# Kernel optimization log

Hardware: AMD Instinct MI355X
Metric: run time of the kernel (lower is better)

## Reference

```python
import jax, jax.numpy as jnp
import numpy as np

NUM_EXPERTS = 8
TOP_K = 2


def setup_inputs() -> dict:
    key = jax.random.key(0)
    ks = jax.random.split(key, 6)
    D, H, E = 1024, 4096, NUM_EXPERTS
    B, S = 4, 2048
    s = 0.02
    return {
        "x": jax.random.normal(ks[0], (B, S, D), jnp.float32),
        "scale_embeddings": jax.random.normal(ks[1], (10, D), jnp.float32) * s,
        "router_w": jax.random.normal(ks[2], (E, D), jnp.float32) * s,
        "router_b": jnp.zeros((E,), jnp.float32),
        "fc1_w": jax.random.normal(ks[3], (E, H, D), jnp.float32) * s,
        "fc1_b": jnp.zeros((E, H), jnp.float32),
        "fc2_w": jax.random.normal(ks[4], (E, D, H), jnp.float32) * s,
        "fc2_b": jnp.zeros((E, D), jnp.float32),
        "scale_idx": 3,
    }


def reference(x, scale_embeddings, router_w, router_b, fc1_w, fc1_b, fc2_w, fc2_b, scale_idx):
    B, S, D = x.shape
    T = B * S
    # Scale-aware router (eval mode: no jitter, temperature=1.0).
    xs = x + scale_embeddings[scale_idx][None, None, :]
    logits = jnp.einsum('bsd,ed->bse', xs, router_w) + router_b  # [B,S,E]
    top_w, top_idx = jax.lax.top_k(logits, TOP_K)                 # [B,S,K]
    top_w = jax.nn.softmax(top_w, axis=-1)

    # Dense per-expert FFN (tanh-approx GELU), then gather top-k expert outputs.
    xf = x.reshape(T, D)
    outs = []
    for e in range(NUM_EXPERTS):
        h = jax.nn.gelu(xf @ fc1_w[e].T + fc1_b[e], approximate=True)  # [T,H]
        outs.append(h @ fc2_w[e].T + fc2_b[e])                          # [T,D]
    all_out = jnp.stack(outs)                                           # [E,T,D]

    idx_f = top_idx.reshape(T, TOP_K)
    w_f = top_w.reshape(T, TOP_K)
    gathered = all_out[idx_f, jnp.arange(T)[:, None]]  # [T,K,D]
    out = (gathered * w_f[..., None]).sum(axis=1)      # [T,D]
    return out.reshape(B, S, D)
```

## Files before the change

### kernel.cpp

```cpp
#include <hip/hip_runtime.h>
#include <math.h>

#define TTOK 8192
#define DDIM 1024
#define HDIM 4096
#define NEXP 8
#define NASSIGN (TTOK * 2)

typedef float f32x4 __attribute__((ext_vector_type(4)));
typedef short s16x8 __attribute__((ext_vector_type(8)));

__device__ __forceinline__ unsigned short f2bf(float f) {
  union { float f; unsigned int u; } v; v.f = f;
  unsigned int u = v.u;
  u += 0x7FFFu + ((u >> 16) & 1u);
  return (unsigned short)(u >> 16);
}

__device__ __forceinline__ float gelu_fast(float x) {
  float u = 0.7978845608028654f * x * (1.0f + 0.044715f * x * x);
  return x / (1.0f + __expf(-2.0f * u));
}

__global__ void cvt_bf16_k(const float* __restrict__ w1, unsigned short* __restrict__ w1b,
                           const float* __restrict__ w2, unsigned short* __restrict__ w2b,
                           int n8) {
  int i = blockIdx.x * blockDim.x + threadIdx.x;
  const float* src; unsigned short* dst;
  if (i < n8) { src = w1; dst = w1b; } else { src = w2; dst = w2b; i -= n8; }
#pragma unroll
  for (int c = 0; c < 2; ++c) {
    float4 v = ((const float4*)src)[i * 2 + c];
    ushort4 o;
    o.x = f2bf(v.x); o.y = f2bf(v.y); o.z = f2bf(v.z); o.w = f2bf(v.w);
    ((ushort4*)dst)[i * 2 + c] = o;
  }
}

__global__ void router_k(const float* __restrict__ x, const float* __restrict__ se,
                         const int* __restrict__ sidx, const float* __restrict__ rw,
                         const float* __restrict__ rb,
                         int* __restrict__ e0, int* __restrict__ e1,
                         float* __restrict__ w0, float* __restrict__ w1,
                         int* __restrict__ counts) {
  int t = blockIdx.x * 4 + (threadIdx.x >> 6);
  int lane = threadIdx.x & 63;
  const float4* xp = (const float4*)(x + (size_t)t * DDIM) + lane * 4;
  const float4* sp = (const float4*)(se + (size_t)sidx[0] * DDIM) + lane * 4;
  float xs[16];
#pragma unroll
  for (int c = 0; c < 4; ++c) {
    float4 a = xp[c], b = sp[c];
    xs[c * 4 + 0] = a.x + b.x; xs[c * 4 + 1] = a.y + b.y;
    xs[c * 4 + 2] = a.z + b.z; xs[c * 4 + 3] = a.w + b.w;
  }
  double acc[NEXP];
#pragma unroll
  for (int e = 0; e < NEXP; ++e) acc[e] = 0.0;
#pragma unroll
  for (int e = 0; e < NEXP; ++e) {
    const float4* wp = (const float4*)(rw + (size_t)e * DDIM) + lane * 4;
#pragma unroll
    for (int c = 0; c < 4; ++c) {
      float4 wv = wp[c];
      acc[e] += (double)xs[c * 4 + 0] * wv.x + (double)xs[c * 4 + 1] * wv.y +
                (double)xs[c * 4 + 2] * wv.z + (double)xs[c * 4 + 3] * wv.w;
    }
  }
#pragma unroll
  for (int e = 0; e < NEXP; ++e) {
#pragma unroll
    for (int m = 32; m >= 1; m >>= 1) acc[e] += __shfl_xor(acc[e], m, 64);
  }
  if (lane == 0) {
    float lg[NEXP];
    for (int e = 0; e < NEXP; ++e) lg[e] = (float)acc[e] + rb[e];
    int i0 = 0; float l0 = lg[0];
    for (int e = 1; e < NEXP; ++e) if (lg[e] > l0) { l0 = lg[e]; i0 = e; }
    int i1 = -1; float l1 = -1e30f;
    for (int e = 0; e < NEXP; ++e) if (e != i0 && lg[e] > l1) { l1 = lg[e]; i1 = e; }
    float z = expf(l1 - l0);
    float p0 = 1.0f / (1.0f + z);
    e0[t] = i0; e1[t] = i1; w0[t] = p0; w1[t] = 1.0f - p0;
    atomicAdd(&counts[i0], 1);
    atomicAdd(&counts[i1], 1);
  }
}

__global__ void scan_k(const int* __restrict__ counts, int* __restrict__ offsets,
                       int* __restrict__ cursors, int4* __restrict__ tileT,
                       int* __restrict__ ntiles) {
  if (threadIdx.x == 0 && blockIdx.x == 0) {
    int s = 0;
    for (int e = 0; e < NEXP; ++e) { offsets[e] = s; cursors[e] = s; s += counts[e]; }
    offsets[NEXP] = s;
    int nt = 0;
    for (int e = 0; e < NEXP; ++e)
      for (int m0 = offsets[e]; m0 < offsets[e + 1]; m0 += 256)
        tileT[nt++] = make_int4(m0, offsets[e + 1], e, 0);
    ntiles[0] = nt;
  }
}

__global__ void scatter_k(const int* __restrict__ e0, const int* __restrict__ e1,
                          const float* __restrict__ w0, const float* __restrict__ w1,
                          int* __restrict__ cursors, int* __restrict__ buckets,
                          float* __restrict__ wts, int* __restrict__ s0,
                          int* __restrict__ s1) {
  int t = blockIdx.x * blockDim.x + threadIdx.x;
  if (t >= TTOK) return;
  int a = e0[t];
  int p = atomicAdd(&cursors[a], 1);
  buckets[p] = t; wts[p] = w0[t]; s0[t] = p;
  a = e1[t];
  p = atomicAdd(&cursors[a], 1);
  buckets[p] = t; wts[p] = w1[t]; s1[t] = p;
}

__global__ void gather_k(const float* __restrict__ x, const int* __restrict__ buckets,
                         unsigned short* __restrict__ Xg) {
  int r = blockIdx.x;
  int t = buckets[r];
  int i = threadIdx.x;
  float4 v = ((const float4*)(x + (size_t)t * DDIM))[i];
  ushort4 o;
  o.x = f2bf(v.x); o.y = f2bf(v.y); o.z = f2bf(v.z); o.w = f2bf(v.w);
  ((ushort4*)(Xg + (size_t)r * DDIM))[i] = o;
}


#define ASP1(p) (const __attribute__((address_space(1))) void*)(p)
#define ASP3(p) (__attribute__((address_space(3))) void*)(p)

#define STAGE_A(KT, H) do {                                                   \
    int kk_ = (KT); if (kk_ >= NKT) kk_ = NKT - 1;                            \
    const int k0_ = kk_ * 64;                                                 \
    unsigned short* d_ = (((KT) & 1) ? LA1 : LA0) + ((H) * 128 + w * 8) * 64; \
    __builtin_amdgcn_global_load_lds(ASP1(aptr[(H) * 2 + 0] + k0_), ASP3(d_), 16, 0, 0);        \
    __builtin_amdgcn_global_load_lds(ASP1(aptr[(H) * 2 + 1] + k0_), ASP3(d_ + 4096), 16, 0, 0); \
  } while (0)

#define STAGE_B(KT, H) do {                                                   \
    int kk_ = (KT); if (kk_ >= NKT) kk_ = NKT - 1;                            \
    const int k0_ = kk_ * 64;                                                 \
    unsigned short* d_ = (((KT) & 1) ? LB1 : LB0) + ((H) * 128 + w * 8) * 64; \
    __builtin_amdgcn_global_load_lds(ASP1(bptr[(H) * 2 + 0] + k0_), ASP3(d_), 16, 0, 0);        \
    __builtin_amdgcn_global_load_lds(ASP1(bptr[(H) * 2 + 1] + k0_), ASP3(d_ + 4096), 16, 0, 0); \
  } while (0)

#define PH(SL, QD, RB, STG) do {                                              \
    if (RB) {                                                                 \
      _Pragma("unroll") for (int nj_ = 0; nj_ < 4; ++nj_)                     \
      _Pragma("unroll") for (int ks_ = 0; ks_ < 2; ++ks_)                     \
        bfrag[nj_][ks_] = *(const s16x8*)(((SL) ? LB1 : LB0) +                \
            (wn * 64 + nj_ * 16 + c16) * 64 + (((ks_ * 4 + q) ^ cx) * 8));    \
    }                                                                         \
    s16x8 afr_[2][2];                                                         \
    _Pragma("unroll") for (int m2_ = 0; m2_ < 2; ++m2_)                       \
    _Pragma("unroll") for (int ks_ = 0; ks_ < 2; ++ks_)                       \
      afr_[m2_][ks_] = *(const s16x8*)(((SL) ? LA1 : LA0) +                   \
          (wm * 128 + ((QD) * 2 + m2_) * 16 + c16) * 64 +                     \
          (((ks_ * 4 + q) ^ cx) * 8));                                        \
    STG;                                                                      \
    asm volatile("s_barrier" ::: "memory");                                   \
    asm volatile("s_waitcnt lgkmcnt(0)" ::: "memory");                        \
    __builtin_amdgcn_sched_barrier(0);                                        \
    __builtin_amdgcn_s_setprio(1);                                            \
    _Pragma("unroll") for (int m2_ = 0; m2_ < 2; ++m2_)                       \
    _Pragma("unroll") for (int nj_ = 0; nj_ < 4; ++nj_)                       \
    _Pragma("unroll") for (int ks_ = 0; ks_ < 2; ++ks_)                       \
      acc[(QD) * 2 + m2_][nj_] = __builtin_amdgcn_mfma_f32_16x16x32_bf16(     \
          afr_[m2_][ks_], bfrag[nj_][ks_], acc[(QD) * 2 + m2_][nj_], 0, 0, 0);\
    __builtin_amdgcn_s_setprio(0);                                            \
  } while (0)

#define BARS asm volatile("s_barrier" ::: "memory")
#define VM4  asm volatile("s_waitcnt vmcnt(4)" ::: "memory")

template <int KD, int ND, int EPI>
__global__ __launch_bounds__(512, 2) void moe_gemm8_k(
    const unsigned short* __restrict__ A,
    const unsigned short* __restrict__ W,
    const float* __restrict__ bias,
    const int4* __restrict__ tileT, const int* __restrict__ ntiles,
    unsigned short* __restrict__ Hout, float* __restrict__ Yout) {
  constexpr int NTN = ND / 256;
  constexpr int NKT = KD / 64;
  extern __shared__ unsigned short lds[];
  unsigned short* const LA0 = lds;
  unsigned short* const LA1 = lds + 16384;
  unsigned short* const LB0 = lds + 32768;
  unsigned short* const LB1 = lds + 49152;

  const int tid = threadIdx.x;
  const int lane = tid & 63;
  const int w = tid >> 6;
  const int wm = w >> 2;
  const int wn = w & 3;
  const int q = lane >> 4;
  const int c16 = lane & 15;
  const int cx = lane & 7;
  const int l8 = lane >> 3;
  const int swz = cx ^ l8;

  const int ntm = ntiles[0];
  const int total = ntm * NTN;
  const int xcd = blockIdx.x & 7;
  const int lid = blockIdx.x >> 3;
  const int bstride = gridDim.x >> 3;
  const int per = (total + 7) >> 3;
  int begin = xcd * per;
  int end = begin + per; if (end > total) end = total;

  for (int idx = begin + lid; idx < end; idx += bstride) {
    const int nb = idx / ntm;
    const int mt = idx - nb * ntm;
    const int4 tl = tileT[mt];
    const int m0 = tl.x, row1 = tl.y, e = tl.z;
    const int n0 = nb * 256;
    const unsigned short* We = W + (size_t)e * ND * KD;

    const unsigned short* aptr[4];
    const unsigned short* bptr[4];
#pragma unroll
    for (int i = 0; i < 4; ++i) {
      int ar = m0 + i * 64 + w * 8 + l8;
      if (ar > row1 - 1) ar = row1 - 1;
      aptr[i] = A + (size_t)ar * KD + swz * 8;
      bptr[i] = We + (size_t)(n0 + i * 64 + w * 8 + l8) * KD + swz * 8;
    }

    f32x4 acc[8][4];
#pragma unroll
    for (int i = 0; i < 8; ++i)
#pragma unroll
      for (int j = 0; j < 4; ++j) acc[i][j] = {0.f, 0.f, 0.f, 0.f};

    s16x8 bfrag[4][2];

    asm volatile("s_waitcnt vmcnt(0)" ::: "memory");
    STAGE_A(0, 0); STAGE_A(0, 1);
    STAGE_B(0, 0); STAGE_B(0, 1);
    STAGE_B(1, 0); STAGE_B(1, 1);
    asm volatile("s_waitcnt vmcnt(4)" ::: "memory");
    asm volatile("s_barrier" ::: "memory");

    for (int it = 0; it < NKT / 2; ++it) {
      const int t2 = 2 * it;
      PH(0, 0, 1, STAGE_A(t2 + 1, 0)); BARS;
      PH(0, 1, 0, STAGE_A(t2 + 1, 1)); BARS;
      PH(0, 2, 0, STAGE_B(t2 + 2, 0)); BARS;
      PH(0, 3, 0, STAGE_B(t2 + 2, 1)); VM4; BARS;
      PH(1, 0, 1, STAGE_A(t2 + 2, 0)); BARS;
      PH(1, 1, 0, STAGE_A(t2 + 2, 1)); BARS;
      PH(1, 2, 0, STAGE_B(t2 + 3, 0)); BARS;
      PH(1, 3, 0, STAGE_B(t2 + 3, 1)); VM4; BARS;
    }

    float bj[4];
#pragma unroll
    for (int nj = 0; nj < 4; ++nj)
      bj[nj] = bias[(size_t)e * ND + n0 + wn * 64 + nj * 16 + c16];
#pragma unroll
    for (int mi = 0; mi < 8; ++mi) {
#pragma unroll
      for (int r = 0; r < 4; ++r) {
        const int m = m0 + wm * 128 + mi * 16 + q * 4 + r;
        if (m < row1) {
#pragma unroll
          for (int nj = 0; nj < 4; ++nj) {
            const int n = n0 + wn * 64 + nj * 16 + c16;
            if (EPI == 0)
              Hout[(size_t)m * ND + n] = f2bf(gelu_fast(acc[mi][nj][r] + bj[nj]));
            else
              Yout[(size_t)m * ND + n] = acc[mi][nj][r] + bj[nj];
          }
        }
      }
    }
  }
}

__global__ void combine_k(const float* __restrict__ Yr, const int* __restrict__ s0,
                          const int* __restrict__ s1, const float* __restrict__ wts,
                          float* __restrict__ out) {
  int t = blockIdx.x;
  int i = threadIdx.x;
  int a = s0[t], b = s1[t];
  float wa = wts[a], wb = wts[b];
  float4 va = ((const float4*)(Yr + (size_t)a * DDIM))[i];
  float4 vb = ((const float4*)(Yr + (size_t)b * DDIM))[i];
  float4 o;
  o.x = wa * va.x + wb * vb.x;
  o.y = wa * va.y + wb * vb.y;
  o.z = wa * va.z + wb * vb.z;
  o.w = wa * va.w + wb * vb.w;
  ((float4*)(out + (size_t)t * DDIM))[i] = o;
}

extern "C" void kernel_launch(void* const* d_in, const int* in_sizes, int n_in,
                              void* d_out, int out_size, void* d_ws, size_t ws_size,
                              hipStream_t stream) {
  const float* x  = (const float*)d_in[0];
  const float* se = (const float*)d_in[1];
  const float* rw = (const float*)d_in[2];
  const float* rb = (const float*)d_in[3];
  const float* w1 = (const float*)d_in[4];
  const float* b1 = (const float*)d_in[5];
  const float* w2 = (const float*)d_in[6];
  const float* b2 = (const float*)d_in[7];
  const int* sidx = (const int*)d_in[8];
  float* out = (float*)d_out;

  char* ws = (char*)d_ws;
  size_t off = 0;
  unsigned short* w1b = (unsigned short*)(ws + off); off += (size_t)NEXP * HDIM * DDIM * 2;
  unsigned short* w2b = (unsigned short*)(ws + off); off += (size_t)NEXP * DDIM * HDIM * 2;
  unsigned short* Xg  = (unsigned short*)(ws + off); off += (size_t)NASSIGN * DDIM * 2;
  unsigned short* Hb  = (unsigned short*)(ws + off); off += (size_t)NASSIGN * HDIM * 2;
  float* Yr = (float*)w1b;
  int*   counts  = (int*)(ws + off); off += 64;
  int*   offsets = (int*)(ws + off); off += 64;
  int*   cursors = (int*)(ws + off); off += 64;
  int*   ntiles  = (int*)(ws + off); off += 64;
  int*   e0  = (int*)(ws + off);   off += (size_t)TTOK * 4;
  int*   e1  = (int*)(ws + off);   off += (size_t)TTOK * 4;
  float* tw0 = (float*)(ws + off); off += (size_t)TTOK * 4;
  float* tw1 = (float*)(ws + off); off += (size_t)TTOK * 4;
  int*   s0  = (int*)(ws + off);   off += (size_t)TTOK * 4;
  int*   s1  = (int*)(ws + off);   off += (size_t)TTOK * 4;
  int*   buckets = (int*)(ws + off); off += (size_t)NASSIGN * 4;
  float* wts = (float*)(ws + off);   off += (size_t)NASSIGN * 4;
  int4*  tileT = (int4*)(ws + off);  off += 256 * 16;

  static int lds_attr_done = 0;
  if (!lds_attr_done) {
    (void)hipFuncSetAttribute((const void*)moe_gemm8_k<DDIM, HDIM, 0>,
                              hipFuncAttributeMaxDynamicSharedMemorySize, 131072);
    (void)hipFuncSetAttribute((const void*)moe_gemm8_k<HDIM, DDIM, 1>,
                              hipFuncAttributeMaxDynamicSharedMemorySize, 131072);
    lds_attr_done = 1;
  }

  hipMemsetAsync(counts, 0, 64, stream);

  const int n8 = NEXP * HDIM * DDIM / 8;
  cvt_bf16_k<<<2 * n8 / 256, 256, 0, stream>>>(w1, w1b, w2, w2b, n8);
  router_k<<<TTOK / 4, 256, 0, stream>>>(x, se, sidx, rw, rb, e0, e1, tw0, tw1, counts);
  scan_k<<<1, 64, 0, stream>>>(counts, offsets, cursors, tileT, ntiles);
  scatter_k<<<TTOK / 256, 256, 0, stream>>>(e0, e1, tw0, tw1, cursors, buckets, wts, s0, s1);
  gather_k<<<NASSIGN, 256, 0, stream>>>(x, buckets, Xg);

  moe_gemm8_k<DDIM, HDIM, 0><<<1024, 512, 131072, stream>>>(Xg, w1b, b1, tileT, ntiles, Hb, Yr);
  moe_gemm8_k<HDIM, DDIM, 1><<<1024, 512, 131072, stream>>>(Hb, w2b, b2, tileT, ntiles, Hb, Yr);
  combine_k<<<TTOK, 256, 0, stream>>>(Yr, s0, s1, wts, out);
}
```

Baseline: 1.034 ms.

## Split-K the second MoE GEMM into two partial buffers summed in combine

The down-projection GEMM (K=4096, N=1024) is split along K into two halves, each writing a separate fp32 partial output, with the combine kernel summing both partials weighted by routing. This raises the tile count for the narrow-N GEMM so more workgroups have work. Both GEMMs now launch with 256 blocks and a fixed stride of 32 instead of 1024 blocks. The weight-conversion kernel also processes one float4 per thread instead of two. The extra partial buffer adds fp32 write and read traffic, and it falls back to no split if the workspace is too small.

```diff
diff --git a/kernel.cpp b/kernel.cpp
--- a/kernel.cpp
+++ b/kernel.cpp
@@ -24,17 +24,14 @@
 
 __global__ void cvt_bf16_k(const float* __restrict__ w1, unsigned short* __restrict__ w1b,
                            const float* __restrict__ w2, unsigned short* __restrict__ w2b,
-                           int n8) {
+                           int n4) {
   int i = blockIdx.x * blockDim.x + threadIdx.x;
   const float* src; unsigned short* dst;
-  if (i < n8) { src = w1; dst = w1b; } else { src = w2; dst = w2b; i -= n8; }
-#pragma unroll
-  for (int c = 0; c < 2; ++c) {
-    float4 v = ((const float4*)src)[i * 2 + c];
-    ushort4 o;
-    o.x = f2bf(v.x); o.y = f2bf(v.y); o.z = f2bf(v.z); o.w = f2bf(v.w);
-    ((ushort4*)dst)[i * 2 + c] = o;
-  }
+  if (i < n4) { src = w1; dst = w1b; } else { src = w2; dst = w2b; i -= n4; }
+  float4 v = ((const float4*)src)[i];
+  ushort4 o;
+  o.x = f2bf(v.x); o.y = f2bf(v.y); o.z = f2bf(v.z); o.w = f2bf(v.w);
+  ((ushort4*)dst)[i] = o;
 }
 
 __global__ void router_k(const float* __restrict__ x, const float* __restrict__ se,
@@ -177,15 +174,17 @@
 #define BARS asm volatile("s_barrier" ::: "memory")
 #define VM4  asm volatile("s_waitcnt vmcnt(4)" ::: "memory")
 
-template <int KD, int ND, int EPI>
+template <int KD, int ND, int EPI, int KSP>
 __global__ __launch_bounds__(512, 2) void moe_gemm8_k(
     const unsigned short* __restrict__ A,
     const unsigned short* __restrict__ W,
     const float* __restrict__ bias,
     const int4* __restrict__ tileT, const int* __restrict__ ntiles,
-    unsigned short* __restrict__ Hout, float* __restrict__ Yout) {
+    unsigned short* __restrict__ Hout, float* __restrict__ Ya,
+    float* __restrict__ Yb) {
   constexpr int NTN = ND / 256;
-  constexpr int NKT = KD / 64;
+  constexpr int KTILE = KD / KSP;
+  constexpr int NKT = KTILE / 64;
   extern __shared__ unsigned short lds[];
   unsigned short* const LA0 = lds;
   unsigned short* const LA1 = lds + 16384;
@@ -204,17 +203,19 @@
   const int swz = cx ^ l8;
 
   const int ntm = ntiles[0];
-  const int total = ntm * NTN;
+  const int total = ntm * NTN * KSP;
   const int xcd = blockIdx.x & 7;
   const int lid = blockIdx.x >> 3;
-  const int bstride = gridDim.x >> 3;
   const int per = (total + 7) >> 3;
   int begin = xcd * per;
   int end = begin + per; if (end > total) end = total;
 
-  for (int idx = begin + lid; idx < end; idx += bstride) {
-    const int nb = idx / ntm;
-    const int mt = idx - nb * ntm;
+  for (int idx = begin + lid; idx < end; idx += 32) {
+    const int nbks = idx / ntm;
+    const int mt = idx - nbks * ntm;
+    const int nb = nbks % NTN;
+    const int ks = nbks / NTN;
+    const int koff = ks * KTILE;
     const int4 tl = tileT[mt];
     const int m0 = tl.x, row1 = tl.y, e = tl.z;
     const int n0 = nb * 256;
@@ -226,8 +227,8 @@
     for (int i = 0; i < 4; ++i) {
       int ar = m0 + i * 64 + w * 8 + l8;
       if (ar > row1 - 1) ar = row1 - 1;
-      aptr[i] = A + (size_t)ar * KD + swz * 8;
-      bptr[i] = We + (size_t)(n0 + i * 64 + w * 8 + l8) * KD + swz * 8;
+      aptr[i] = A + (size_t)ar * KD + koff + swz * 8;
+      bptr[i] = We + (size_t)(n0 + i * 64 + w * 8 + l8) * KD + koff + swz * 8;
     }
 
     f32x4 acc[8][4];
@@ -257,10 +258,13 @@
       PH(1, 3, 0, STAGE_B(t2 + 3, 1)); VM4; BARS;
     }
 
+    float* const Yp = (KSP > 1 && ks != 0) ? Yb : Ya;
     float bj[4];
 #pragma unroll
-    for (int nj = 0; nj < 4; ++nj)
+    for (int nj = 0; nj < 4; ++nj) {
       bj[nj] = bias[(size_t)e * ND + n0 + wn * 64 + nj * 16 + c16];
+      if (KSP > 1 && ks != 0) bj[nj] = 0.f;
+    }
 #pragma unroll
     for (int mi = 0; mi < 8; ++mi) {
 #pragma unroll
@@ -273,7 +277,7 @@
             if (EPI == 0)
               Hout[(size_t)m * ND + n] = f2bf(gelu_fast(acc[mi][nj][r] + bj[nj]));
             else
-              Yout[(size_t)m * ND + n] = acc[mi][nj][r] + bj[nj];
+              Yp[(size_t)m * ND + n] = acc[mi][nj][r] + bj[nj];
           }
         }
       }
@@ -281,20 +285,28 @@
   }
 }
 
-__global__ void combine_k(const float* __restrict__ Yr, const int* __restrict__ s0,
-                          const int* __restrict__ s1, const float* __restrict__ wts,
-                          float* __restrict__ out) {
+__global__ void combine_k(const float* __restrict__ Ya, const float* __restrict__ Yb,
+                          const int* __restrict__ s0, const int* __restrict__ s1,
+                          const float* __restrict__ wts, float* __restrict__ out) {
   int t = blockIdx.x;
   int i = threadIdx.x;
   int a = s0[t], b = s1[t];
   float wa = wts[a], wb = wts[b];
-  float4 va = ((const float4*)(Yr + (size_t)a * DDIM))[i];
-  float4 vb = ((const float4*)(Yr + (size_t)b * DDIM))[i];
+  float4 va = ((const float4*)(Ya + (size_t)a * DDIM))[i];
+  float4 vb = ((const float4*)(Ya + (size_t)b * DDIM))[i];
   float4 o;
   o.x = wa * va.x + wb * vb.x;
   o.y = wa * va.y + wb * vb.y;
   o.z = wa * va.z + wb * vb.z;
   o.w = wa * va.w + wb * vb.w;
+  if (Yb != nullptr) {
+    float4 ua = ((const float4*)(Yb + (size_t)a * DDIM))[i];
+    float4 ub = ((const float4*)(Yb + (size_t)b * DDIM))[i];
+    o.x += wa * ua.x + wb * ub.x;
+    o.y += wa * ua.y + wb * ub.y;
+    o.z += wa * ua.z + wb * ub.z;
+    o.w += wa * ua.w + wb * ub.w;
+  }
   ((float4*)(out + (size_t)t * DDIM))[i] = o;
 }
 
@@ -333,25 +345,37 @@
   float* wts = (float*)(ws + off);   off += (size_t)NASSIGN * 4;
   int4*  tileT = (int4*)(ws + off);  off += 256 * 16;
 
+  size_t yb_bytes = (size_t)NASSIGN * DDIM * 4;
+  float* Yb = nullptr;
+  if (ws_size >= off + yb_bytes) { Yb = (float*)(ws + off); off += yb_bytes; }
+
   static int lds_attr_done = 0;
   if (!lds_attr_done) {
-    (void)hipFuncSetAttribute((const void*)moe_gemm8_k<DDIM, HDIM, 0>,
+    (void)hipFuncSetAttribute((const void*)moe_gemm8_k<DDIM, HDIM, 0, 1>,
                               hipFuncAttributeMaxDynamicSharedMemorySize, 131072);
-    (void)hipFuncSetAttribute((const void*)moe_gemm8_k<HDIM, DDIM, 1>,
+    (void)hipFuncSetAttribute((const void*)moe_gemm8_k<HDIM, DDIM, 1, 2>,
+                              hipFuncAttributeMaxDynamicSharedMemorySize, 131072);
+    (void)hipFuncSetAttribute((const void*)moe_gemm8_k<HDIM, DDIM, 1, 1>,
                               hipFuncAttributeMaxDynamicSharedMemorySize, 131072);
     lds_attr_done = 1;
   }
 
   hipMemsetAsync(counts, 0, 64, stream);
 
-  const int n8 = NEXP * HDIM * DDIM / 8;
-  cvt_bf16_k<<<2 * n8 / 256, 256, 0, stream>>>(w1, w1b, w2, w2b, n8);
+  const int n4 = NEXP * HDIM * DDIM / 4;
+  cvt_bf16_k<<<2 * n4 / 256, 256, 0, stream>>>(w1, w1b, w2, w2b, n4);
   router_k<<<TTOK / 4, 256, 0, stream>>>(x, se, sidx, rw, rb, e0, e1, tw0, tw1, counts);
   scan_k<<<1, 64, 0, stream>>>(counts, offsets, cursors, tileT, ntiles);
   scatter_k<<<TTOK / 256, 256, 0, stream>>>(e0, e1, tw0, tw1, cursors, buckets, wts, s0, s1);
   gather_k<<<NASSIGN, 256, 0, stream>>>(x, buckets, Xg);
 
-  moe_gemm8_k<DDIM, HDIM, 0><<<1024, 512, 131072, stream>>>(Xg, w1b, b1, tileT, ntiles, Hb, Yr);
-  moe_gemm8_k<HDIM, DDIM, 1><<<1024, 512, 131072, stream>>>(Hb, w2b, b2, tileT, ntiles, Hb, Yr);
-  combine_k<<<TTOK, 256, 0, stream>>>(Yr, s0, s1, wts, out);
-}
+  moe_gemm8_k<DDIM, HDIM, 0, 1><<<256, 512, 131072, stream>>>(
+      Xg, w1b, b1, tileT, ntiles, Hb, Yr, nullptr);
+  if (Yb != nullptr)
+    moe_gemm8_k<HDIM, DDIM, 1, 2><<<256, 512, 131072, stream>>>(
+        Hb, w2b, b2, tileT, ntiles, Hb, Yr, Yb);
+  else
+    moe_gemm8_k<HDIM, DDIM, 1, 1><<<256, 512, 131072, stream>>>(
+        Hb, w2b, b2, tileT, ntiles, Hb, Yr, nullptr);
+  combine_k<<<TTOK, 256, 0, stream>>>(Yr, Yb, s0, s1, wts, out);
+}
```

Result: faster. 995.7 us (-3.7%).
